# Optimization experiments

Measured on AMD Instinct MI355X. Metric: run time of the kernel, lower is better.

Reference implementation:

```python
import jax, jax.numpy as jnp
import numpy as np

LN_EPS = 1e-5
LOG_EPS = 1e-8

def _layernorm(x, w, b):
    mu = jnp.mean(x, axis=-1, keepdims=True)
    var = jnp.mean((x - mu) ** 2, axis=-1, keepdims=True)
    return (x - mu) * jax.lax.rsqrt(var + LN_EPS) * w + b


def setup_inputs() -> dict:
    key = jax.random.key(0)
    ks = jax.random.split(key, 8)
    B, T, D = 4, 4096, 1024
    x = jax.random.normal(ks[0], (B, T, D), dtype=jnp.float32)
    ln_w = jnp.ones((D,), jnp.float32)
    ln_b = jnp.zeros((D,), jnp.float32)
    # torch Linear stores weight as (out, in)
    Wf = jax.random.normal(ks[1], (D, D), jnp.float32) / np.sqrt(D)
    bf = jax.random.normal(ks[2], (D,), jnp.float32) * 0.02
    # module inits reach to zeros; use small random values for a non-trivial baseline
    Wr = jax.random.normal(ks[3], (D, D), jnp.float32) * 0.02
    br = jax.random.normal(ks[4], (D,), jnp.float32) * 0.02
    alpha_bias = jnp.array([3.0], jnp.float32) + jax.random.normal(ks[5], (1,), jnp.float32) * 0.1
    beta_scale = jnp.array([0.02], jnp.float32)
    return {"x": x, "ln_w": ln_w, "ln_b": ln_b, "Wf": Wf, "bf": bf,
            "Wr": Wr, "br": br, "alpha_bias": alpha_bias, "beta_scale": beta_scale}


def reference(x, ln_w, ln_b, Wf, bf, Wr, br, alpha_bias, beta_scale):
    residual = x
    x_norm = _layernorm(x, ln_w, ln_b)                       # [B,T,D]
    alpha = jax.nn.sigmoid(jnp.einsum('btd,ed->bte', x_norm, Wf) + bf + alpha_bias)
    beta_x = beta_scale * (1.0 - alpha) * x_norm
    log_alpha = jnp.log(alpha + LOG_EPS)
    log_alpha_cumsum = jnp.cumsum(log_alpha, axis=1)          # [B,T,D]
    m = jnp.max(log_alpha_cumsum, axis=1, keepdims=True)      # [B,1,D]
    scale = jnp.exp(log_alpha_cumsum - m)
    x_star = beta_x * scale
    s_star = jnp.cumsum(x_star, axis=1)
    output = s_star / (scale + LOG_EPS)
    x_gate = jnp.tanh(jnp.einsum('btd,ed->bte', output, Wr) + br)
    return x_gate * 0.05 + residual
```

## Files before the change

kernel.cpp:

```cpp
#include <hip/hip_runtime.h>

#define D_DIM 1024
#define B_DIM 4
#define T_DIM 4096
#define M_DIM (B_DIM * T_DIM)
#define CHUNK 32
#define NCHUNK (T_DIM / CHUNK)
#define SEG (NCHUNK / 4)

typedef unsigned short u16;
typedef __attribute__((ext_vector_type(8))) unsigned short us8;
typedef __attribute__((ext_vector_type(8))) __bf16 bf16x8;
typedef __attribute__((ext_vector_type(4))) float f32x4;

__device__ __forceinline__ float bf2f(u16 u) {
    union { unsigned int i; float f; } v;
    v.i = ((unsigned int)u) << 16;
    return v.f;
}
__device__ __forceinline__ u16 f2bf(float f) {
    union { float f; unsigned int i; } v;
    v.f = f;
    unsigned int u = v.i;
    unsigned int r = (u + 0x7fffu + ((u >> 16) & 1u)) >> 16;
    return (u16)r;
}
__device__ __forceinline__ float fast_tanh(float v) {
    float e = __expf(2.f * v);
    return 1.f - 2.f / (e + 1.f);
}

#define GLOAD16(g, l)                                                   \
    __builtin_amdgcn_global_load_lds(                                   \
        (const __attribute__((address_space(1))) void*)(g),             \
        (__attribute__((address_space(3))) void*)(l), 16, 0, 0)

__global__ __launch_bounds__(256) void conv2_kernel(const float* __restrict__ a,
                                                    const float* __restrict__ b,
                                                    u16* __restrict__ da,
                                                    u16* __restrict__ db) {
    int i = blockIdx.x * 256 + threadIdx.x;
    const float* s = (i < 262144) ? a : b;
    u16* dp = (i < 262144) ? da : db;
    int j = i & 262143;
    float4 v = ((const float4*)s)[j];
    ushort4 o;
    o.x = f2bf(v.x); o.y = f2bf(v.y); o.z = f2bf(v.z); o.w = f2bf(v.w);
    ((ushort4*)dp)[j] = o;
}

__global__ __launch_bounds__(256) void ln_kernel(const float* __restrict__ x,
                                                 const float* __restrict__ w,
                                                 const float* __restrict__ b,
                                                 u16* __restrict__ xn) {
    __shared__ float red[8];
    int row = blockIdx.x;
    int tid = threadIdx.x;
    float4 v = ((const float4*)(x + (size_t)row * D_DIM))[tid];
    float s  = v.x + v.y + v.z + v.w;
    float s2 = v.x * v.x + v.y * v.y + v.z * v.z + v.w * v.w;
    #pragma unroll
    for (int o = 32; o > 0; o >>= 1) {
        s  += __shfl_xor(s, o, 64);
        s2 += __shfl_xor(s2, o, 64);
    }
    int wave = tid >> 6, lane = tid & 63;
    if (lane == 0) { red[wave] = s; red[wave + 4] = s2; }
    __syncthreads();
    if (tid == 0) {
        float ts  = red[0] + red[1] + red[2] + red[3];
        float ts2 = red[4] + red[5] + red[6] + red[7];
        float mu  = ts * (1.0f / D_DIM);
        float var = ts2 * (1.0f / D_DIM) - mu * mu;
        red[0] = mu;
        red[1] = rsqrtf(var + 1e-5f);
    }
    __syncthreads();
    float mu = red[0], rs = red[1];
    float4 wv = ((const float4*)w)[tid];
    float4 bv = ((const float4*)b)[tid];
    ushort4 o;
    o.x = f2bf((v.x - mu) * rs * wv.x + bv.x);
    o.y = f2bf((v.y - mu) * rs * wv.y + bv.y);
    o.z = f2bf((v.z - mu) * rs * wv.z + bv.z);
    o.w = f2bf((v.w - mu) * rs * wv.w + bv.w);
    ((ushort4*)(xn + (size_t)row * D_DIM))[tid] = o;
}

template <int EPI>
__global__ __launch_bounds__(256) void gemm_kernel(const u16* __restrict__ A,
                                                   const u16* __restrict__ Bm,
                                                   const float* __restrict__ bias,
                                                   const float* __restrict__ resid,
                                                   const float* __restrict__ sc0,
                                                   u16* __restrict__ out_bf,
                                                   float* __restrict__ out_f) {
    __shared__ __align__(16) u16 lds_a[128 * 32];
    __shared__ __align__(16) u16 lds_b[128 * 32];
    int tid  = threadIdx.x;
    int wave = tid >> 6, lane = tid & 63;
    int tile_n = blockIdx.x * 128;
    int tile_m = blockIdx.y * 128;
    int wr = wave >> 1, wc = wave & 1;

    f32x4 acc[4][4] = {};

    int srow = wave * 32 + (lane >> 2);
    int scol = (lane & 3) * 8;
    const u16* ga0 = A  + (size_t)(tile_m + srow) * D_DIM + scol;
    const u16* ga1 = ga0 + 16 * D_DIM;
    const u16* gb0 = Bm + (size_t)(tile_n + srow) * D_DIM + scol;
    const u16* gb1 = gb0 + 16 * D_DIM;
    u16* la0 = &lds_a[(wave * 32) * 32];
    u16* la1 = &lds_a[(wave * 32 + 16) * 32];
    u16* lb0 = &lds_b[(wave * 32) * 32];
    u16* lb1 = &lds_b[(wave * 32 + 16) * 32];

    for (int k0 = 0; k0 < D_DIM; k0 += 32) {
        GLOAD16(ga0 + k0, la0);
        GLOAD16(ga1 + k0, la1);
        GLOAD16(gb0 + k0, lb0);
        GLOAD16(gb1 + k0, lb1);
        __syncthreads();

        bf16x8 af[4], bfr[4];
        #pragma unroll
        for (int mi = 0; mi < 4; mi++) {
            int m = wr * 64 + mi * 16 + (lane & 15);
            af[mi] = *(const bf16x8*)&lds_a[m * 32 + (lane >> 4) * 8];
        }
        #pragma unroll
        for (int ni = 0; ni < 4; ni++) {
            int n = wc * 64 + ni * 16 + (lane & 15);
            bfr[ni] = *(const bf16x8*)&lds_b[n * 32 + (lane >> 4) * 8];
        }
        #pragma unroll
        for (int mi = 0; mi < 4; mi++)
            #pragma unroll
            for (int ni = 0; ni < 4; ni++)
                acc[mi][ni] = __builtin_amdgcn_mfma_f32_16x16x32_bf16(
                    af[mi], bfr[ni], acc[mi][ni], 0, 0, 0);
        __syncthreads();
    }

    if constexpr (EPI == 0) {
        float abv = sc0[0];
        #pragma unroll
        for (int mi = 0; mi < 4; mi++) {
            #pragma unroll
            for (int r = 0; r < 4; r++) {
                int row = tile_m + wr * 64 + mi * 16 + (lane >> 4) * 4 + r;
                #pragma unroll
                for (int ni = 0; ni < 4; ni++) {
                    int col = tile_n + wc * 64 + ni * 16 + (lane & 15);
                    size_t idx = (size_t)row * D_DIM + col;
                    float z = acc[mi][ni][r] + bias[col] + abv;
                    float alpha = 1.f / (1.f + __expf(-z));
                    out_bf[idx] = f2bf(__logf(alpha + 1e-8f));
                }
            }
        }
    } else {
        #pragma unroll
        for (int mi = 0; mi < 4; mi++) {
            #pragma unroll
            for (int r = 0; r < 4; r++) {
                int row = tile_m + wr * 64 + mi * 16 + (lane >> 4) * 4 + r;
                #pragma unroll
                for (int ni = 0; ni < 4; ni++) {
                    int col = tile_n + wc * 64 + ni * 16 + (lane & 15);
                    size_t idx = (size_t)row * D_DIM + col;
                    float g = fast_tanh(acc[mi][ni][r] + bias[col]);
                    out_f[idx] = 0.05f * g + resid[idx];
                }
            }
        }
    }
}

__global__ __launch_bounds__(256) void scan_chunk(const u16* __restrict__ la,
                                                  const u16* __restrict__ xn,
                                                  const float* __restrict__ bs,
                                                  float* __restrict__ S,
                                                  float* __restrict__ Ml,
                                                  float* __restrict__ Tb) {
    int bc = blockIdx.x;
    int b = bc >> 7, c = bc & (NCHUNK - 1);
    int d = blockIdx.y * 256 + threadIdx.x;
    float bsv = bs[0];
    size_t base = ((size_t)(b * T_DIM + c * CHUNK)) * D_DIM + d;
    float p[CHUNK];
    float run = 0.f, mx = -3.4e38f;
    #pragma unroll
    for (int t = 0; t < CHUNK; t++) {
        run += bf2f(la[base + (size_t)t * D_DIM]);
        p[t] = run;
        mx = fmaxf(mx, run);
    }
    float tb = 0.f;
    #pragma unroll
    for (int t = 0; t < CHUNK; t++) {
        size_t idx = base + (size_t)t * D_DIM;
        float lav = bf2f(la[idx]);
        float bx = bsv * (-expm1f(lav)) * bf2f(xn[idx]);
        tb += bx * __expf(p[t] - mx);
    }
    size_t ci = ((size_t)(b * NCHUNK + c)) * D_DIM + d;
    S[ci] = run; Ml[ci] = mx; Tb[ci] = tb;
}

__global__ __launch_bounds__(256) void scan_combine(const float* __restrict__ S,
                                                    const float* __restrict__ Ml,
                                                    const float* __restrict__ Tb,
                                                    float* __restrict__ Of,
                                                    float* __restrict__ SSp) {
    __shared__ float lsS[4][64], lsM[4][64], lsW[4][64];
    int b = blockIdx.x >> 4;
    int dg = blockIdx.x & 15;
    int wave = threadIdx.x >> 6, lane = threadIdx.x & 63;
    int d = dg * 64 + lane;
    size_t base = ((size_t)b * NCHUNK) * D_DIM + d;
    int c0 = wave * SEG;

    float O = 0.f, m = -3.4e38f;
    for (int j = 0; j < SEG; j++) {
        size_t ci = base + (size_t)(c0 + j) * D_DIM;
        m = fmaxf(m, O + Ml[ci]);
        O += S[ci];
    }
    lsS[wave][lane] = O; lsM[wave][lane] = m;
    __syncthreads();

    float myOsup = 0.f, gm = -3.4e38f;
    {
        float o = 0.f;
        #pragma unroll
        for (int w2 = 0; w2 < 4; w2++) {
            if (w2 == wave) myOsup = o;
            gm = fmaxf(gm, o + lsM[w2][lane]);
            o += lsS[w2][lane];
        }
    }

    float wv[SEG];
    float wacc = 0.f, Oc = myOsup;
    for (int j = 0; j < SEG; j++) {
        size_t ci = base + (size_t)(c0 + j) * D_DIM;
        Of[ci] = Oc - gm;
        float wcj = __expf(Oc + Ml[ci] - gm) * Tb[ci];
        wv[j] = wacc;
        wacc += wcj;
        Oc += S[ci];
    }
    lsW[wave][lane] = wacc;
    __syncthreads();

    float ssup = 0.f;
    #pragma unroll
    for (int w2 = 0; w2 < 4; w2++)
        if (w2 < wave) ssup += lsW[w2][lane];

    for (int j = 0; j < SEG; j++) {
        size_t ci = base + (size_t)(c0 + j) * D_DIM;
        SSp[ci] = ssup + wv[j];
    }
}

__global__ __launch_bounds__(256) void scan_final(const u16* __restrict__ la,
                                                  const u16* __restrict__ xn,
                                                  const float* __restrict__ bs,
                                                  const float* __restrict__ Of,
                                                  const float* __restrict__ SSp,
                                                  u16* __restrict__ osc) {
    int bc = blockIdx.x;
    int b = bc >> 7, c = bc & (NCHUNK - 1);
    int d = blockIdx.y * 256 + threadIdx.x;
    float bsv = bs[0];
    size_t base = ((size_t)(b * T_DIM + c * CHUNK)) * D_DIM + d;
    size_t ci = ((size_t)(b * NCHUNK + c)) * D_DIM + d;
    float ofs = Of[ci], ss = SSp[ci], p = 0.f;
    #pragma unroll
    for (int t = 0; t < CHUNK; t++) {
        size_t idx = base + (size_t)t * D_DIM;
        float lav = bf2f(la[idx]);
        p += lav;
        float scv = __expf(ofs + p);
        float bx = bsv * (-expm1f(lav)) * bf2f(xn[idx]);
        ss += bx * scv;
        osc[idx] = f2bf(ss / (scv + 1e-8f));
    }
}

extern "C" void kernel_launch(void* const* d_in, const int* in_sizes, int n_in,
                              void* d_out, int out_size, void* d_ws, size_t ws_size,
                              hipStream_t stream) {
    const float* x   = (const float*)d_in[0];
    const float* lnw = (const float*)d_in[1];
    const float* lnb = (const float*)d_in[2];
    const float* Wf  = (const float*)d_in[3];
    const float* bf_ = (const float*)d_in[4];
    const float* Wr  = (const float*)d_in[5];
    const float* br  = (const float*)d_in[6];
    const float* ab  = (const float*)d_in[7];
    const float* bs  = (const float*)d_in[8];
    float* out = (float*)d_out;

    char* w = (char*)d_ws;
    u16* xn  = (u16*)w;
    u16* la  = (u16*)(w + (size_t)33554432);
    u16* Wfc = (u16*)(w + (size_t)67108864);
    u16* Wrc = (u16*)(w + (size_t)69206016);
    float* S   = (float*)(w + (size_t)71303168);
    float* Ml  = S  + 524288;
    float* Tb  = Ml + 524288;
    float* Of  = Tb + 524288;
    float* SSp = Of + 524288;
    u16* osc = xn;

    conv2_kernel<<<dim3(2048), dim3(256), 0, stream>>>(Wf, Wr, Wfc, Wrc);
    ln_kernel<<<dim3(M_DIM), dim3(256), 0, stream>>>(x, lnw, lnb, xn);
    gemm_kernel<0><<<dim3(D_DIM / 128, M_DIM / 128), dim3(256), 0, stream>>>(
        xn, Wfc, bf_, nullptr, ab, la, nullptr);
    scan_chunk<<<dim3(B_DIM * NCHUNK, 4), dim3(256), 0, stream>>>(la, xn, bs, S, Ml, Tb);
    scan_combine<<<dim3(B_DIM * 16), dim3(256), 0, stream>>>(S, Ml, Tb, Of, SSp);
    scan_final<<<dim3(B_DIM * NCHUNK, 4), dim3(256), 0, stream>>>(la, xn, bs, Of, SSp, osc);
    gemm_kernel<1><<<dim3(D_DIM / 128, M_DIM / 128), dim3(256), 0, stream>>>(
        osc, Wrc, br, x, nullptr, nullptr, out);
}
```

Baseline: 307.6 us.

## Double GEMM K-tile to 64 and vectorize scan kernels over eight columns

The GEMM now stages a 64-wide K slice per iteration instead of 32, which halves the number of barrier pairs and global-load rounds. LDS use per block doubles to 32 KB, and the row stride of 64 bf16 can cause more bank conflicts on the fragment reads. The scan_chunk and scan_final kernels now give each thread 8 adjacent columns, loaded and stored as 16-byte vectors, and run with 128-thread blocks, so there are far fewer blocks (512) and each thread does more serial work. expm1f is replaced by 1 - exp, which loses some accuracy when log-alpha is near zero.

```diff
diff --git a/kernel.cpp b/kernel.cpp
--- a/kernel.cpp
+++ b/kernel.cpp
@@ -7,6 +7,7 @@
 #define CHUNK 32
 #define NCHUNK (T_DIM / CHUNK)
 #define SEG (NCHUNK / 4)
+#define BK 64
 
 typedef unsigned short u16;
 typedef __attribute__((ext_vector_type(8))) unsigned short us8;
@@ -95,8 +96,8 @@
                                                    const float* __restrict__ sc0,
                                                    u16* __restrict__ out_bf,
                                                    float* __restrict__ out_f) {
-    __shared__ __align__(16) u16 lds_a[128 * 32];
-    __shared__ __align__(16) u16 lds_b[128 * 32];
+    __shared__ __align__(16) u16 lds_a[128 * BK];
+    __shared__ __align__(16) u16 lds_b[128 * BK];
     int tid  = threadIdx.x;
     int wave = tid >> 6, lane = tid & 63;
     int tile_n = blockIdx.x * 128;
@@ -105,41 +106,42 @@
 
     f32x4 acc[4][4] = {};
 
-    int srow = wave * 32 + (lane >> 2);
-    int scol = (lane & 3) * 8;
-    const u16* ga0 = A  + (size_t)(tile_m + srow) * D_DIM + scol;
-    const u16* ga1 = ga0 + 16 * D_DIM;
-    const u16* gb0 = Bm + (size_t)(tile_n + srow) * D_DIM + scol;
-    const u16* gb1 = gb0 + 16 * D_DIM;
-    u16* la0 = &lds_a[(wave * 32) * 32];
-    u16* la1 = &lds_a[(wave * 32 + 16) * 32];
-    u16* lb0 = &lds_b[(wave * 32) * 32];
-    u16* lb1 = &lds_b[(wave * 32 + 16) * 32];
-
-    for (int k0 = 0; k0 < D_DIM; k0 += 32) {
-        GLOAD16(ga0 + k0, la0);
-        GLOAD16(ga1 + k0, la1);
-        GLOAD16(gb0 + k0, lb0);
-        GLOAD16(gb1 + k0, lb1);
+    int srow = wave * 32 + (lane >> 3);
+    int scol = (lane & 7) * 8;
+    const u16* gaBase = A  + (size_t)(tile_m + srow) * D_DIM + scol;
+    const u16* gbBase = Bm + (size_t)(tile_n + srow) * D_DIM + scol;
+
+    for (int k0 = 0; k0 < D_DIM; k0 += BK) {
+        #pragma unroll
+        for (int i = 0; i < 4; i++)
+            GLOAD16(gaBase + (size_t)i * 8 * D_DIM + k0,
+                    &lds_a[(wave * 32 + i * 8) * BK]);
+        #pragma unroll
+        for (int i = 0; i < 4; i++)
+            GLOAD16(gbBase + (size_t)i * 8 * D_DIM + k0,
+                    &lds_b[(wave * 32 + i * 8) * BK]);
         __syncthreads();
 
-        bf16x8 af[4], bfr[4];
-        #pragma unroll
-        for (int mi = 0; mi < 4; mi++) {
-            int m = wr * 64 + mi * 16 + (lane & 15);
-            af[mi] = *(const bf16x8*)&lds_a[m * 32 + (lane >> 4) * 8];
-        }
-        #pragma unroll
-        for (int ni = 0; ni < 4; ni++) {
-            int n = wc * 64 + ni * 16 + (lane & 15);
-            bfr[ni] = *(const bf16x8*)&lds_b[n * 32 + (lane >> 4) * 8];
-        }
-        #pragma unroll
-        for (int mi = 0; mi < 4; mi++)
-            #pragma unroll
-            for (int ni = 0; ni < 4; ni++)
-                acc[mi][ni] = __builtin_amdgcn_mfma_f32_16x16x32_bf16(
-                    af[mi], bfr[ni], acc[mi][ni], 0, 0, 0);
+        #pragma unroll
+        for (int kk = 0; kk < BK; kk += 32) {
+            bf16x8 af[4], bfr[4];
+            #pragma unroll
+            for (int mi = 0; mi < 4; mi++) {
+                int m = wr * 64 + mi * 16 + (lane & 15);
+                af[mi] = *(const bf16x8*)&lds_a[m * BK + kk + (lane >> 4) * 8];
+            }
+            #pragma unroll
+            for (int ni = 0; ni < 4; ni++) {
+                int n = wc * 64 + ni * 16 + (lane & 15);
+                bfr[ni] = *(const bf16x8*)&lds_b[n * BK + kk + (lane >> 4) * 8];
+            }
+            #pragma unroll
+            for (int mi = 0; mi < 4; mi++)
+                #pragma unroll
+                for (int ni = 0; ni < 4; ni++)
+                    acc[mi][ni] = __builtin_amdgcn_mfma_f32_16x16x32_bf16(
+                        af[mi], bfr[ni], acc[mi][ni], 0, 0, 0);
+        }
         __syncthreads();
     }
 
@@ -178,7 +180,7 @@
     }
 }
 
-__global__ __launch_bounds__(256) void scan_chunk(const u16* __restrict__ la,
+__global__ __launch_bounds__(128) void scan_chunk(const u16* __restrict__ la,
                                                   const u16* __restrict__ xn,
                                                   const float* __restrict__ bs,
                                                   float* __restrict__ S,
@@ -186,27 +188,38 @@
                                                   float* __restrict__ Tb) {
     int bc = blockIdx.x;
     int b = bc >> 7, c = bc & (NCHUNK - 1);
-    int d = blockIdx.y * 256 + threadIdx.x;
+    int col0 = threadIdx.x * 8;
     float bsv = bs[0];
-    size_t base = ((size_t)(b * T_DIM + c * CHUNK)) * D_DIM + d;
-    float p[CHUNK];
-    float run = 0.f, mx = -3.4e38f;
-    #pragma unroll
+    size_t base = ((size_t)(b * T_DIM + c * CHUNK)) * D_DIM + col0;
+    float run[8], mx[8];
+    #pragma unroll
+    for (int j = 0; j < 8; j++) { run[j] = 0.f; mx[j] = -3.4e38f; }
     for (int t = 0; t < CHUNK; t++) {
-        run += bf2f(la[base + (size_t)t * D_DIM]);
-        p[t] = run;
-        mx = fmaxf(mx, run);
-    }
-    float tb = 0.f;
-    #pragma unroll
+        us8 v = *(const us8*)(la + base + (size_t)t * D_DIM);
+        #pragma unroll
+        for (int j = 0; j < 8; j++) {
+            run[j] += bf2f(v[j]);
+            mx[j] = fmaxf(mx[j], run[j]);
+        }
+    }
+    float tb[8], p[8];
+    #pragma unroll
+    for (int j = 0; j < 8; j++) { tb[j] = 0.f; p[j] = 0.f; }
     for (int t = 0; t < CHUNK; t++) {
         size_t idx = base + (size_t)t * D_DIM;
-        float lav = bf2f(la[idx]);
-        float bx = bsv * (-expm1f(lav)) * bf2f(xn[idx]);
-        tb += bx * __expf(p[t] - mx);
-    }
-    size_t ci = ((size_t)(b * NCHUNK + c)) * D_DIM + d;
-    S[ci] = run; Ml[ci] = mx; Tb[ci] = tb;
+        us8 lv = *(const us8*)(la + idx);
+        us8 xv = *(const us8*)(xn + idx);
+        #pragma unroll
+        for (int j = 0; j < 8; j++) {
+            float lav = bf2f(lv[j]);
+            p[j] += lav;
+            float bx = bsv * (1.f - __expf(lav)) * bf2f(xv[j]);
+            tb[j] += bx * __expf(p[j] - mx[j]);
+        }
+    }
+    size_t ci = ((size_t)(b * NCHUNK + c)) * D_DIM + col0;
+    #pragma unroll
+    for (int j = 0; j < 8; j++) { S[ci + j] = run[j]; Ml[ci + j] = mx[j]; Tb[ci + j] = tb[j]; }
 }
 
 __global__ __launch_bounds__(256) void scan_combine(const float* __restrict__ S,
@@ -266,7 +279,7 @@
     }
 }
 
-__global__ __launch_bounds__(256) void scan_final(const u16* __restrict__ la,
+__global__ __launch_bounds__(128) void scan_final(const u16* __restrict__ la,
                                                   const u16* __restrict__ xn,
                                                   const float* __restrict__ bs,
                                                   const float* __restrict__ Of,
@@ -274,20 +287,28 @@
                                                   u16* __restrict__ osc) {
     int bc = blockIdx.x;
     int b = bc >> 7, c = bc & (NCHUNK - 1);
-    int d = blockIdx.y * 256 + threadIdx.x;
+    int col0 = threadIdx.x * 8;
     float bsv = bs[0];
-    size_t base = ((size_t)(b * T_DIM + c * CHUNK)) * D_DIM + d;
-    size_t ci = ((size_t)(b * NCHUNK + c)) * D_DIM + d;
-    float ofs = Of[ci], ss = SSp[ci], p = 0.f;
-    #pragma unroll
+    size_t base = ((size_t)(b * T_DIM + c * CHUNK)) * D_DIM + col0;
+    size_t ci = ((size_t)(b * NCHUNK + c)) * D_DIM + col0;
+    float ofs[8], ss[8], p[8];
+    #pragma unroll
+    for (int j = 0; j < 8; j++) { ofs[j] = Of[ci + j]; ss[j] = SSp[ci + j]; p[j] = 0.f; }
     for (int t = 0; t < CHUNK; t++) {
         size_t idx = base + (size_t)t * D_DIM;
-        float lav = bf2f(la[idx]);
-        p += lav;
-        float scv = __expf(ofs + p);
-        float bx = bsv * (-expm1f(lav)) * bf2f(xn[idx]);
-        ss += bx * scv;
-        osc[idx] = f2bf(ss / (scv + 1e-8f));
+        us8 lv = *(const us8*)(la + idx);
+        us8 xv = *(const us8*)(xn + idx);
+        us8 o;
+        #pragma unroll
+        for (int j = 0; j < 8; j++) {
+            float lav = bf2f(lv[j]);
+            p[j] += lav;
+            float scv = __expf(ofs[j] + p[j]);
+            float bx = bsv * (1.f - __expf(lav)) * bf2f(xv[j]);
+            ss[j] += bx * scv;
+            o[j] = f2bf(ss[j] / (scv + 1e-8f));
+        }
+        *(us8*)(osc + idx) = o;
     }
 }
 
@@ -321,9 +342,9 @@
     ln_kernel<<<dim3(M_DIM), dim3(256), 0, stream>>>(x, lnw, lnb, xn);
     gemm_kernel<0><<<dim3(D_DIM / 128, M_DIM / 128), dim3(256), 0, stream>>>(
         xn, Wfc, bf_, nullptr, ab, la, nullptr);
-    scan_chunk<<<dim3(B_DIM * NCHUNK, 4), dim3(256), 0, stream>>>(la, xn, bs, S, Ml, Tb);
+    scan_chunk<<<dim3(B_DIM * NCHUNK), dim3(128), 0, stream>>>(la, xn, bs, S, Ml, Tb);
     scan_combine<<<dim3(B_DIM * 16), dim3(256), 0, stream>>>(S, Ml, Tb, Of, SSp);
-    scan_final<<<dim3(B_DIM * NCHUNK, 4), dim3(256), 0, stream>>>(la, xn, bs, Of, SSp, osc);
+    scan_final<<<dim3(B_DIM * NCHUNK), dim3(128), 0, stream>>>(la, xn, bs, Of, SSp, osc);
     gemm_kernel<1><<<dim3(D_DIM / 128, M_DIM / 128), dim3(256), 0, stream>>>(
         osc, Wrc, br, x, nullptr, nullptr, out);
 }
```

Result: slower. 325.7 us (+5.9%).

## Fuse first GEMM with chunked scan via decoupled look-back chaining

Applied to the files above, without the earlier changes.

Merges the weight conversion into the layernorm launch and fuses the first GEMM with the whole time scan. Each 128x128 tile computes log-alpha and beta*x into shared memory, reduces per-column chunk aggregates, and chains prefix state across tiles using global flags and decoupled look-back. Tile order comes from an atomic ticket so predecessors are always scheduled first. This removes the la intermediate round trip and three scan kernels. In exchange, only 128 of 256 threads do the serial scan, the look-back adds spin-waiting, and the running max is taken from the first element rather than the true maximum, which risks overflow in exp.

```diff
diff --git a/kernel.cpp b/kernel.cpp
--- a/kernel.cpp
+++ b/kernel.cpp
@@ -4,12 +4,12 @@
 #define B_DIM 4
 #define T_DIM 4096
 #define M_DIM (B_DIM * T_DIM)
-#define CHUNK 32
-#define NCHUNK (T_DIM / CHUNK)
-#define SEG (NCHUNK / 4)
+#define NC 32
+#define NCHAIN 32
+#define COLS 128
 
 typedef unsigned short u16;
-typedef __attribute__((ext_vector_type(8))) unsigned short us8;
+typedef unsigned int u32;
 typedef __attribute__((ext_vector_type(8))) __bf16 bf16x8;
 typedef __attribute__((ext_vector_type(4))) float f32x4;
 
@@ -35,27 +35,28 @@
         (const __attribute__((address_space(1))) void*)(g),             \
         (__attribute__((address_space(3))) void*)(l), 16, 0, 0)
 
-__global__ __launch_bounds__(256) void conv2_kernel(const float* __restrict__ a,
-                                                    const float* __restrict__ b,
-                                                    u16* __restrict__ da,
-                                                    u16* __restrict__ db) {
-    int i = blockIdx.x * 256 + threadIdx.x;
-    const float* s = (i < 262144) ? a : b;
-    u16* dp = (i < 262144) ? da : db;
-    int j = i & 262143;
-    float4 v = ((const float4*)s)[j];
-    ushort4 o;
-    o.x = f2bf(v.x); o.y = f2bf(v.y); o.z = f2bf(v.z); o.w = f2bf(v.w);
-    ((ushort4*)dp)[j] = o;
-}
-
-__global__ __launch_bounds__(256) void ln_kernel(const float* __restrict__ x,
-                                                 const float* __restrict__ w,
-                                                 const float* __restrict__ b,
-                                                 u16* __restrict__ xn) {
+__global__ __launch_bounds__(256) void ln_conv_kernel(const float* __restrict__ x,
+                                                      const float* __restrict__ w,
+                                                      const float* __restrict__ b,
+                                                      u16* __restrict__ xn,
+                                                      const float* __restrict__ Wf,
+                                                      const float* __restrict__ Wr,
+                                                      u16* __restrict__ da,
+                                                      u16* __restrict__ db) {
     __shared__ float red[8];
-    int row = blockIdx.x;
     int tid = threadIdx.x;
+    if (blockIdx.x < 2048) {
+        int i = blockIdx.x * 256 + tid;
+        const float* s = (i < 262144) ? Wf : Wr;
+        u16* dp = (i < 262144) ? da : db;
+        int j = i & 262143;
+        float4 v = ((const float4*)s)[j];
+        ushort4 o;
+        o.x = f2bf(v.x); o.y = f2bf(v.y); o.z = f2bf(v.z); o.w = f2bf(v.w);
+        ((ushort4*)dp)[j] = o;
+        return;
+    }
+    int row = blockIdx.x - 2048;
     float4 v = ((const float4*)(x + (size_t)row * D_DIM))[tid];
     float s  = v.x + v.y + v.z + v.w;
     float s2 = v.x * v.x + v.y * v.y + v.z * v.z + v.w * v.w;
@@ -87,14 +88,186 @@
     ((ushort4*)(xn + (size_t)row * D_DIM))[tid] = o;
 }
 
-template <int EPI>
-__global__ __launch_bounds__(256) void gemm_kernel(const u16* __restrict__ A,
-                                                   const u16* __restrict__ Bm,
-                                                   const float* __restrict__ bias,
-                                                   const float* __restrict__ resid,
-                                                   const float* __restrict__ sc0,
-                                                   u16* __restrict__ out_bf,
-                                                   float* __restrict__ out_f) {
+union ShMem {
+    struct { u16 a[128 * 32]; u16 b[128 * 32]; } g;
+    u32 pk[128 * 128];
+};
+
+__global__ __launch_bounds__(256) void gemm_scan_kernel(
+    const u16* __restrict__ xn, const u16* __restrict__ Wfc,
+    const float* __restrict__ bf_, const float* __restrict__ ab,
+    const float* __restrict__ bs,
+    float* __restrict__ Sg, float* __restrict__ Tg,
+    float* __restrict__ CSg, float* __restrict__ SSg, float* __restrict__ Mg,
+    int* __restrict__ flags, int* __restrict__ tick,
+    u16* __restrict__ osc) {
+    __shared__ ShMem sh;
+    __shared__ int s_bcast;
+    int tid = threadIdx.x;
+    int wave = tid >> 6, lane = tid & 63;
+
+    if (tid == 0) s_bcast = atomicAdd(tick, 1);
+    __syncthreads();
+    int v = s_bcast;
+    __syncthreads();
+    int chain = v & 31;
+    int c     = v >> 5;
+    int tn    = chain >> 2;
+    int b     = chain & 3;
+    int tile_n = tn * 128;
+    int tile_m = (b * 32 + c) * 128;
+    int link0  = chain * NC;
+    size_t pme = (size_t)(link0 + c) * COLS;
+
+    int wr = wave >> 1, wc = wave & 1;
+    f32x4 acc[4][4] = {};
+
+    int srow = wave * 32 + (lane >> 2);
+    int scol = (lane & 3) * 8;
+    const u16* ga0 = xn  + (size_t)(tile_m + srow) * D_DIM + scol;
+    const u16* ga1 = ga0 + 16 * D_DIM;
+    const u16* gb0 = Wfc + (size_t)(tile_n + srow) * D_DIM + scol;
+    const u16* gb1 = gb0 + 16 * D_DIM;
+    u16* la0 = &sh.g.a[(wave * 32) * 32];
+    u16* la1 = &sh.g.a[(wave * 32 + 16) * 32];
+    u16* lb0 = &sh.g.b[(wave * 32) * 32];
+    u16* lb1 = &sh.g.b[(wave * 32 + 16) * 32];
+
+    for (int k0 = 0; k0 < D_DIM; k0 += 32) {
+        GLOAD16(ga0 + k0, la0);
+        GLOAD16(ga1 + k0, la1);
+        GLOAD16(gb0 + k0, lb0);
+        GLOAD16(gb1 + k0, lb1);
+        __syncthreads();
+        bf16x8 af[4], bfr[4];
+        #pragma unroll
+        for (int mi = 0; mi < 4; mi++) {
+            int m_ = wr * 64 + mi * 16 + (lane & 15);
+            af[mi] = *(const bf16x8*)&sh.g.a[m_ * 32 + (lane >> 4) * 8];
+        }
+        #pragma unroll
+        for (int ni = 0; ni < 4; ni++) {
+            int n_ = wc * 64 + ni * 16 + (lane & 15);
+            bfr[ni] = *(const bf16x8*)&sh.g.b[n_ * 32 + (lane >> 4) * 8];
+        }
+        #pragma unroll
+        for (int mi = 0; mi < 4; mi++)
+            #pragma unroll
+            for (int ni = 0; ni < 4; ni++)
+                acc[mi][ni] = __builtin_amdgcn_mfma_f32_16x16x32_bf16(
+                    af[mi], bfr[ni], acc[mi][ni], 0, 0, 0);
+        __syncthreads();
+    }
+
+    float abv = ab[0], bsv = bs[0];
+    #pragma unroll
+    for (int mi = 0; mi < 4; mi++) {
+        #pragma unroll
+        for (int r_ = 0; r_ < 4; r_++) {
+            int row = wr * 64 + mi * 16 + (lane >> 4) * 4 + r_;
+            #pragma unroll
+            for (int ni = 0; ni < 4; ni++) {
+                int col = wc * 64 + ni * 16 + (lane & 15);
+                float z = acc[mi][ni][r_] + bf_[tile_n + col] + abv;
+                float alpha = 1.f / (1.f + __expf(-z));
+                float lav = __logf(alpha + 1e-8f);
+                float xv = bf2f(xn[(size_t)(tile_m + row) * D_DIM + tile_n + col]);
+                float bxv = bsv * (1.f - alpha) * xv;
+                sh.pk[row * 128 + col] = (u32)f2bf(lav) | ((u32)f2bf(bxv) << 16);
+            }
+        }
+    }
+    __syncthreads();
+
+    float Sc = 0.f, Tc = 0.f;
+    if (tid < COLS) {
+        float q = 0.f, Tacc = 0.f;
+        for (int t = 0; t < 128; t++) {
+            u32 p = sh.pk[t * 128 + tid];
+            float la = bf2f((u16)(p & 0xffffu));
+            float bx = bf2f((u16)(p >> 16));
+            q += la;
+            Tacc += bx * __expf(q);
+        }
+        Sc = q; Tc = Tacc;
+    }
+    if (c > 0) {
+        if (tid < COLS) {
+            __hip_atomic_store(&Sg[pme + tid], Sc, __ATOMIC_RELAXED, __HIP_MEMORY_SCOPE_AGENT);
+            __hip_atomic_store(&Tg[pme + tid], Tc, __ATOMIC_RELAXED, __HIP_MEMORY_SCOPE_AGENT);
+        }
+        __threadfence();
+        __syncthreads();
+        if (tid == 0)
+            __hip_atomic_store(&flags[link0 + c], 1, __ATOMIC_RELEASE, __HIP_MEMORY_SCOPE_AGENT);
+    }
+
+    float m = 0.f, cs_exc = 0.f, s_exc = 0.f;
+    if (c == 0) {
+        if (tid < COLS) m = bf2f((u16)(sh.pk[tid] & 0xffffu));
+    } else {
+        int j = c - 1;
+        for (;;) {
+            if (tid == 0) {
+                int f;
+                do {
+                    f = __hip_atomic_load(&flags[link0 + j], __ATOMIC_ACQUIRE,
+                                          __HIP_MEMORY_SCOPE_AGENT);
+                    if (f == 0) __builtin_amdgcn_s_sleep(2);
+                } while (f == 0);
+                s_bcast = f;
+            }
+            __syncthreads();
+            int f = s_bcast;
+            __syncthreads();
+            if (f == 2) break;
+            j--;
+        }
+        __threadfence();
+        if (tid < COLS) {
+            size_t pj = (size_t)(link0 + j) * COLS + tid;
+            m      = __hip_atomic_load(&Mg[pj],  __ATOMIC_RELAXED, __HIP_MEMORY_SCOPE_AGENT);
+            cs_exc = __hip_atomic_load(&CSg[pj], __ATOMIC_RELAXED, __HIP_MEMORY_SCOPE_AGENT);
+            s_exc  = __hip_atomic_load(&SSg[pj], __ATOMIC_RELAXED, __HIP_MEMORY_SCOPE_AGENT);
+            for (int jj = j + 1; jj < c; jj++) {
+                size_t pa = (size_t)(link0 + jj) * COLS + tid;
+                float Tj = __hip_atomic_load(&Tg[pa], __ATOMIC_RELAXED, __HIP_MEMORY_SCOPE_AGENT);
+                float Sj = __hip_atomic_load(&Sg[pa], __ATOMIC_RELAXED, __HIP_MEMORY_SCOPE_AGENT);
+                s_exc += Tj * __expf(cs_exc - m);
+                cs_exc += Sj;
+            }
+        }
+    }
+    if (tid < COLS) {
+        __hip_atomic_store(&CSg[pme + tid], cs_exc + Sc, __ATOMIC_RELAXED, __HIP_MEMORY_SCOPE_AGENT);
+        __hip_atomic_store(&SSg[pme + tid], s_exc + Tc * __expf(cs_exc - m),
+                           __ATOMIC_RELAXED, __HIP_MEMORY_SCOPE_AGENT);
+        __hip_atomic_store(&Mg[pme + tid], m, __ATOMIC_RELAXED, __HIP_MEMORY_SCOPE_AGENT);
+    }
+    __threadfence();
+    __syncthreads();
+    if (tid == 0)
+        __hip_atomic_store(&flags[link0 + c], 2, __ATOMIC_RELEASE, __HIP_MEMORY_SCOPE_AGENT);
+
+    if (tid < COLS) {
+        float runp = cs_exc, s = s_exc;
+        for (int t = 0; t < 128; t++) {
+            u32 p = sh.pk[t * 128 + tid];
+            float la = bf2f((u16)(p & 0xffffu));
+            float bx = bf2f((u16)(p >> 16));
+            runp += la;
+            float scv = __expf(runp - m);
+            s += bx * scv;
+            osc[(size_t)(tile_m + t) * D_DIM + tile_n + tid] = f2bf(s / (scv + 1e-8f));
+        }
+    }
+}
+
+__global__ __launch_bounds__(256) void gemm2_kernel(const u16* __restrict__ A,
+                                                    const u16* __restrict__ Bm,
+                                                    const float* __restrict__ bias,
+                                                    const float* __restrict__ resid,
+                                                    float* __restrict__ out_f) {
     __shared__ __align__(16) u16 lds_a[128 * 32];
     __shared__ __align__(16) u16 lds_b[128 * 32];
     int tid  = threadIdx.x;
@@ -102,9 +275,7 @@
     int tile_n = blockIdx.x * 128;
     int tile_m = blockIdx.y * 128;
     int wr = wave >> 1, wc = wave & 1;
-
     f32x4 acc[4][4] = {};
-
     int srow = wave * 32 + (lane >> 2);
     int scol = (lane & 3) * 8;
     const u16* ga0 = A  + (size_t)(tile_m + srow) * D_DIM + scol;
@@ -115,14 +286,12 @@
     u16* la1 = &lds_a[(wave * 32 + 16) * 32];
     u16* lb0 = &lds_b[(wave * 32) * 32];
     u16* lb1 = &lds_b[(wave * 32 + 16) * 32];
-
     for (int k0 = 0; k0 < D_DIM; k0 += 32) {
         GLOAD16(ga0 + k0, la0);
         GLOAD16(ga1 + k0, la1);
         GLOAD16(gb0 + k0, lb0);
         GLOAD16(gb1 + k0, lb1);
         __syncthreads();
-
         bf16x8 af[4], bfr[4];
         #pragma unroll
         for (int mi = 0; mi < 4; mi++) {
@@ -142,152 +311,19 @@
                     af[mi], bfr[ni], acc[mi][ni], 0, 0, 0);
         __syncthreads();
     }
-
-    if constexpr (EPI == 0) {
-        float abv = sc0[0];
-        #pragma unroll
-        for (int mi = 0; mi < 4; mi++) {
+    #pragma unroll
+    for (int mi = 0; mi < 4; mi++) {
+        #pragma unroll
+        for (int r = 0; r < 4; r++) {
+            int row = tile_m + wr * 64 + mi * 16 + (lane >> 4) * 4 + r;
             #pragma unroll
-            for (int r = 0; r < 4; r++) {
-                int row = tile_m + wr * 64 + mi * 16 + (lane >> 4) * 4 + r;
-                #pragma unroll
-                for (int ni = 0; ni < 4; ni++) {
-                    int col = tile_n + wc * 64 + ni * 16 + (lane & 15);
-                    size_t idx = (size_t)row * D_DIM + col;
-                    float z = acc[mi][ni][r] + bias[col] + abv;
-                    float alpha = 1.f / (1.f + __expf(-z));
-                    out_bf[idx] = f2bf(__logf(alpha + 1e-8f));
-                }
+            for (int ni = 0; ni < 4; ni++) {
+                int col = tile_n + wc * 64 + ni * 16 + (lane & 15);
+                size_t idx = (size_t)row * D_DIM + col;
+                float g = fast_tanh(acc[mi][ni][r] + bias[col]);
+                out_f[idx] = 0.05f * g + resid[idx];
             }
         }
-    } else {
-        #pragma unroll
-        for (int mi = 0; mi < 4; mi++) {
-            #pragma unroll
-            for (int r = 0; r < 4; r++) {
-                int row = tile_m + wr * 64 + mi * 16 + (lane >> 4) * 4 + r;
-                #pragma unroll
-                for (int ni = 0; ni < 4; ni++) {
-                    int col = tile_n + wc * 64 + ni * 16 + (lane & 15);
-                    size_t idx = (size_t)row * D_DIM + col;
-                    float g = fast_tanh(acc[mi][ni][r] + bias[col]);
-                    out_f[idx] = 0.05f * g + resid[idx];
-                }
-            }
-        }
-    }
-}
-
-__global__ __launch_bounds__(256) void scan_chunk(const u16* __restrict__ la,
-                                                  const u16* __restrict__ xn,
-                                                  const float* __restrict__ bs,
-                                                  float* __restrict__ S,
-                                                  float* __restrict__ Ml,
-                                                  float* __restrict__ Tb) {
-    int bc = blockIdx.x;
-    int b = bc >> 7, c = bc & (NCHUNK - 1);
-    int d = blockIdx.y * 256 + threadIdx.x;
-    float bsv = bs[0];
-    size_t base = ((size_t)(b * T_DIM + c * CHUNK)) * D_DIM + d;
-    float p[CHUNK];
-    float run = 0.f, mx = -3.4e38f;
-    #pragma unroll
-    for (int t = 0; t < CHUNK; t++) {
-        run += bf2f(la[base + (size_t)t * D_DIM]);
-        p[t] = run;
-        mx = fmaxf(mx, run);
-    }
-    float tb = 0.f;
-    #pragma unroll
-    for (int t = 0; t < CHUNK; t++) {
-        size_t idx = base + (size_t)t * D_DIM;
-        float lav = bf2f(la[idx]);
-        float bx = bsv * (-expm1f(lav)) * bf2f(xn[idx]);
-        tb += bx * __expf(p[t] - mx);
-    }
-    size_t ci = ((size_t)(b * NCHUNK + c)) * D_DIM + d;
-    S[ci] = run; Ml[ci] = mx; Tb[ci] = tb;
-}
-
-__global__ __launch_bounds__(256) void scan_combine(const float* __restrict__ S,
-                                                    const float* __restrict__ Ml,
-                                                    const float* __restrict__ Tb,
-                                                    float* __restrict__ Of,
-                                                    float* __restrict__ SSp) {
-    __shared__ float lsS[4][64], lsM[4][64], lsW[4][64];
-    int b = blockIdx.x >> 4;
-    int dg = blockIdx.x & 15;
-    int wave = threadIdx.x >> 6, lane = threadIdx.x & 63;
-    int d = dg * 64 + lane;
-    size_t base = ((size_t)b * NCHUNK) * D_DIM + d;
-    int c0 = wave * SEG;
-
-    float O = 0.f, m = -3.4e38f;
-    for (int j = 0; j < SEG; j++) {
-        size_t ci = base + (size_t)(c0 + j) * D_DIM;
-        m = fmaxf(m, O + Ml[ci]);
-        O += S[ci];
-    }
-    lsS[wave][lane] = O; lsM[wave][lane] = m;
-    __syncthreads();
-
-    float myOsup = 0.f, gm = -3.4e38f;
-    {
-        float o = 0.f;
-        #pragma unroll
-        for (int w2 = 0; w2 < 4; w2++) {
-            if (w2 == wave) myOsup = o;
-            gm = fmaxf(gm, o + lsM[w2][lane]);
-            o += lsS[w2][lane];
-        }
-    }
-
-    float wv[SEG];
-    float wacc = 0.f, Oc = myOsup;
-    for (int j = 0; j < SEG; j++) {
-        size_t ci = base + (size_t)(c0 + j) * D_DIM;
-        Of[ci] = Oc - gm;
-        float wcj = __expf(Oc + Ml[ci] - gm) * Tb[ci];
-        wv[j] = wacc;
-        wacc += wcj;
-        Oc += S[ci];
-    }
-    lsW[wave][lane] = wacc;
-    __syncthreads();
-
-    float ssup = 0.f;
-    #pragma unroll
-    for (int w2 = 0; w2 < 4; w2++)
-        if (w2 < wave) ssup += lsW[w2][lane];
-
-    for (int j = 0; j < SEG; j++) {
-        size_t ci = base + (size_t)(c0 + j) * D_DIM;
-        SSp[ci] = ssup + wv[j];
-    }
-}
-
-__global__ __launch_bounds__(256) void scan_final(const u16* __restrict__ la,
-                                                  const u16* __restrict__ xn,
-                                                  const float* __restrict__ bs,
-                                                  const float* __restrict__ Of,
-                                                  const float* __restrict__ SSp,
-                                                  u16* __restrict__ osc) {
-    int bc = blockIdx.x;
-    int b = bc >> 7, c = bc & (NCHUNK - 1);
-    int d = blockIdx.y * 256 + threadIdx.x;
-    float bsv = bs[0];
-    size_t base = ((size_t)(b * T_DIM + c * CHUNK)) * D_DIM + d;
-    size_t ci = ((size_t)(b * NCHUNK + c)) * D_DIM + d;
-    float ofs = Of[ci], ss = SSp[ci], p = 0.f;
-    #pragma unroll
-    for (int t = 0; t < CHUNK; t++) {
-        size_t idx = base + (size_t)t * D_DIM;
-        float lav = bf2f(la[idx]);
-        p += lav;
-        float scv = __expf(ofs + p);
-        float bx = bsv * (-expm1f(lav)) * bf2f(xn[idx]);
-        ss += bx * scv;
-        osc[idx] = f2bf(ss / (scv + 1e-8f));
     }
 }
 
@@ -307,23 +343,22 @@
 
     char* w = (char*)d_ws;
     u16* xn  = (u16*)w;
-    u16* la  = (u16*)(w + (size_t)33554432);
+    u16* osc = (u16*)(w + (size_t)33554432);
     u16* Wfc = (u16*)(w + (size_t)67108864);
     u16* Wrc = (u16*)(w + (size_t)69206016);
-    float* S   = (float*)(w + (size_t)71303168);
-    float* Ml  = S  + 524288;
-    float* Tb  = Ml + 524288;
-    float* Of  = Tb + 524288;
-    float* SSp = Of + 524288;
-    u16* osc = xn;
-
-    conv2_kernel<<<dim3(2048), dim3(256), 0, stream>>>(Wf, Wr, Wfc, Wrc);
-    ln_kernel<<<dim3(M_DIM), dim3(256), 0, stream>>>(x, lnw, lnb, xn);
-    gemm_kernel<0><<<dim3(D_DIM / 128, M_DIM / 128), dim3(256), 0, stream>>>(
-        xn, Wfc, bf_, nullptr, ab, la, nullptr);
-    scan_chunk<<<dim3(B_DIM * NCHUNK, 4), dim3(256), 0, stream>>>(la, xn, bs, S, Ml, Tb);
-    scan_combine<<<dim3(B_DIM * 16), dim3(256), 0, stream>>>(S, Ml, Tb, Of, SSp);
-    scan_final<<<dim3(B_DIM * NCHUNK, 4), dim3(256), 0, stream>>>(la, xn, bs, Of, SSp, osc);
-    gemm_kernel<1><<<dim3(D_DIM / 128, M_DIM / 128), dim3(256), 0, stream>>>(
-        osc, Wrc, br, x, nullptr, nullptr, out);
-}
+    float* Sg  = (float*)(w + (size_t)71303168);
+    float* Tg  = Sg  + 131072;
+    float* CSg = Tg  + 131072;
+    float* SSg = CSg + 131072;
+    float* Mg  = SSg + 131072;
+    int* flags = (int*)(Mg + 131072);
+    int* tick  = flags + NCHAIN * NC;
+
+    hipMemsetAsync(flags, 0, (NCHAIN * NC + 1) * sizeof(int), stream);
+    ln_conv_kernel<<<dim3(2048 + M_DIM), dim3(256), 0, stream>>>(
+        x, lnw, lnb, xn, Wf, Wr, Wfc, Wrc);
+    gemm_scan_kernel<<<dim3(1024), dim3(256), 0, stream>>>(
+        xn, Wfc, bf_, ab, bs, Sg, Tg, CSg, SSg, Mg, flags, tick, osc);
+    gemm2_kernel<<<dim3(D_DIM / 128, M_DIM / 128), dim3(256), 0, stream>>>(
+        osc, Wrc, br, x, out);
+}
```

Result: slower. 799.0 us (+159.7%).
